# Kernel optimization log

Hardware: AMD Instinct MI355X
Metric: run time of the kernel (lower is better)

Reference implementation:

```python
import jax, jax.numpy as jnp
import numpy as np

DIM = 1024
FF = 4096
BATCH = 4
SEQ = 2048
EPS = 1e-5


def setup_inputs() -> dict:
    key = jax.random.key(0)
    ks = jax.random.split(key, 8)
    x = jax.random.normal(ks[0], (BATCH, SEQ, DIM), dtype=jnp.float32)
    # phazor init: exp(2j*pi*arange(dim)/dim) * |randn(dim)|
    ang = 2.0 * np.pi * jnp.arange(DIM, dtype=jnp.float32) / DIM
    mag = jnp.abs(jax.random.normal(ks[1], (DIM,), dtype=jnp.float32))
    phazor_re = mag * jnp.cos(ang)
    phazor_im = mag * jnp.sin(ang)
    last_re = jax.random.normal(ks[2], (DIM,), dtype=jnp.float32)
    last_im = jax.random.normal(ks[3], (DIM,), dtype=jnp.float32)
    w1 = jax.random.normal(ks[4], (FF, DIM), dtype=jnp.float32) * DIM ** -0.5
    b1 = jnp.zeros((FF,), dtype=jnp.float32)
    w2 = jax.random.normal(ks[5], (DIM, FF), dtype=jnp.float32) * FF ** -0.5
    b2 = jnp.zeros((DIM,), dtype=jnp.float32)
    return {
        'x': x,
        'ln1_w': jnp.ones((DIM,), jnp.float32), 'ln1_b': jnp.zeros((DIM,), jnp.float32),
        'ln2_w': jnp.ones((DIM,), jnp.float32), 'ln2_b': jnp.zeros((DIM,), jnp.float32),
        'sc_lin': jnp.ones((DIM,), jnp.float32),
        'phazor_re': phazor_re, 'phazor_im': phazor_im,
        'last_re': last_re, 'last_im': last_im,
        'w1': w1, 'b1': b1, 'w2': w2, 'b2': b2,
    }


def _layer_norm(x, w, b):
    mu = jnp.mean(x, axis=-1, keepdims=True)
    var = jnp.mean(jnp.square(x - mu), axis=-1, keepdims=True)
    return (x - mu) * jax.lax.rsqrt(var + EPS) * w + b


def _sconv(x, phazor_re, phazor_im, last_re, last_im):
    B, L, D = x.shape
    dtype = x.dtype
    xc = x.astype(jnp.complex64)
    p_raw = phazor_re + 1j * phazor_im
    # tanh(|p|) * exp(i*angle(p))
    p = (jnp.tanh(jnp.abs(p_raw)) * jnp.exp(1j * jnp.angle(p_raw))).astype(jnp.complex64)
    t = jnp.arange(L)[:, None]
    prog = jnp.power(p[None, :], t)            # [L, D] complex
    filt_fft = jnp.fft.fft(prog, n=2 * L, axis=0)   # [2L, D]
    x_fft = jnp.fft.fft(xc, n=2 * L, axis=1)        # [B, 2L, D]
    conv = jnp.fft.ifft(filt_fft[None] * x_fft, axis=1)[:, :L]  # [B, L, D]
    last = (last_re + 1j * last_im)[None, None, :]  # [1,1,D] broadcast over batch
    conv_with_past = conv + last * prog[None] * p[None, None]
    return conv_with_past.real.astype(dtype)


def reference(x, ln1_w, ln1_b, ln2_w, ln2_b, sc_lin,
              phazor_re, phazor_im, last_re, last_im,
              w1, b1, w2, b2):
    # SConv branch
    x_res = x
    h = _layer_norm(x, ln1_w, ln1_b)
    h = jax.nn.silu(h)
    h = _sconv(h, phazor_re, phazor_im, last_re, last_im)
    h = h * sc_lin
    x = h + x_res
    # FFN branch
    x_res = x
    h = _layer_norm(x, ln2_w, ln2_b)
    h = jax.nn.silu(jnp.einsum('bld,fd->blf', h, w1) + b1)
    h = jnp.einsum('blf,df->bld', h, w2) + b2
    return h + x_res
```

## Files before the change

### kernel.cpp

```cpp
#include <hip/hip_runtime.h>
#include <cmath>


#define DIMD 1024
#define FFD  4096
#define BATCH 4
#define SEQL 2048
#define MROWS (BATCH*SEQL)
#define EPSF 1e-5f
#define CHUNKS 32
#define CLEN (SEQL/CHUNKS)

typedef __attribute__((ext_vector_type(8))) _Float16 half8;
typedef __attribute__((ext_vector_type(4))) _Float16 half4;
typedef __attribute__((ext_vector_type(4))) float    floatx4;

#define H_OFF    0u
#define E_OFF    33554432u
#define SIN_OFF  34603008u
#define H2_OFF   35651584u
#define W1H_OFF  52428800u
#define W2H_OFF  60817408u
#define Y1_OFF   69206016u

__device__ __forceinline__ void load_lds16(const _Float16* g, _Float16* l) {
    __builtin_amdgcn_global_load_lds(
        (const __attribute__((address_space(1))) unsigned int*)g,
        (__attribute__((address_space(3))) unsigned int*)l,
        16, 0, 0);
}

__global__ __launch_bounds__(256)
void cast_f32_f16(const float* __restrict__ src, _Float16* __restrict__ dst) {
    int i = (blockIdx.x * 256 + threadIdx.x) * 4;
    float4 v = *(const float4*)(src + i);
    half4 o;
    o.x = (_Float16)v.x; o.y = (_Float16)v.y; o.z = (_Float16)v.z; o.w = (_Float16)v.w;
    *(half4*)(dst + i) = o;
}

__global__ __launch_bounds__(256)
void ln_kernel(const float* __restrict__ x, const float* __restrict__ w,
               const float* __restrict__ b, float* __restrict__ of,
               _Float16* __restrict__ oh, int mode) {
    const size_t row = blockIdx.x;
    const int tid = threadIdx.x;
    float4 v = *(const float4*)(x + row * DIMD + tid * 4);
    float s = (v.x + v.y) + (v.z + v.w);
    float q = (v.x * v.x + v.y * v.y) + (v.z * v.z + v.w * v.w);
    #pragma unroll
    for (int off = 32; off; off >>= 1) {
        s += __shfl_down(s, off, 64);
        q += __shfl_down(q, off, 64);
    }
    __shared__ float red[8];
    if (!(tid & 63)) { red[tid >> 6] = s; red[4 + (tid >> 6)] = q; }
    __syncthreads();
    s = (red[0] + red[1]) + (red[2] + red[3]);
    q = (red[4] + red[5]) + (red[6] + red[7]);
    const float mu = s * (1.f / DIMD);
    const float rs = rsqrtf(q * (1.f / DIMD) - mu * mu + EPSF);
    float4 wv = *(const float4*)(w + tid * 4);
    float4 bv = *(const float4*)(b + tid * 4);
    float o0 = (v.x - mu) * rs * wv.x + bv.x;
    float o1 = (v.y - mu) * rs * wv.y + bv.y;
    float o2 = (v.z - mu) * rs * wv.z + bv.z;
    float o3 = (v.w - mu) * rs * wv.w + bv.w;
    if (mode == 1) {
        o0 = o0 / (1.f + __expf(-o0));
        o1 = o1 / (1.f + __expf(-o1));
        o2 = o2 / (1.f + __expf(-o2));
        o3 = o3 / (1.f + __expf(-o3));
        float4 ov = {o0, o1, o2, o3};
        *(float4*)(of + row * DIMD + tid * 4) = ov;
    } else {
        half4 hv;
        hv.x = (_Float16)o0; hv.y = (_Float16)o1;
        hv.z = (_Float16)o2; hv.w = (_Float16)o3;
        *(half4*)(oh + row * DIMD + tid * 4) = hv;
    }
}

__device__ __forceinline__ void get_p(const float* pre, const float* pim, int d,
                                      float& pr, float& pi) {
    float re = pre[d], im = pim[d];
    float r = sqrtf(re * re + im * im);
    float t = tanhf(r) / fmaxf(r, 1e-30f);
    pr = re * t; pi = im * t;
}

__global__ __launch_bounds__(256)
void scan_partial(const float* __restrict__ h, const float* __restrict__ pre,
                  const float* __restrict__ pim, float2* __restrict__ e) {
    const int d = blockIdx.x * 256 + threadIdx.x;
    const int c = blockIdx.y;
    const int bb = blockIdx.z;
    float pr, pi; get_p(pre, pim, d, pr, pi);
    float sr = 0.f, si = 0.f;
    const float* hp = h + ((size_t)bb * SEQL + (size_t)c * CLEN) * DIMD + d;
    #pragma unroll 4
    for (int j = 0; j < CLEN; ++j) {
        float hv = hp[(size_t)j * DIMD];
        float nr = pr * sr - pi * si + hv;
        float ni = pr * si + pi * sr;
        sr = nr; si = ni;
    }
    e[((size_t)bb * CHUNKS + c) * DIMD + d] = make_float2(sr, si);
}

__global__ __launch_bounds__(256)
void scan_combine(const float2* __restrict__ e, const float* __restrict__ pre,
                  const float* __restrict__ pim, const float* __restrict__ lre,
                  const float* __restrict__ lim, float2* __restrict__ sv) {
    const int d = blockIdx.x * 256 + threadIdx.x;
    const int bb = blockIdx.y;
    float pr, pi; get_p(pre, pim, d, pr, pi);
    float qr = pr, qi = pi;
    #pragma unroll
    for (int s = 0; s < 6; ++s) {
        float nr = qr * qr - qi * qi;
        float ni = 2.f * qr * qi;
        qr = nr; qi = ni;
    }
    float sr = lre[d], si = lim[d];
    for (int c = 0; c < CHUNKS; ++c) {
        sv[((size_t)bb * CHUNKS + c) * DIMD + d] = make_float2(sr, si);
        float2 ec = e[((size_t)bb * CHUNKS + c) * DIMD + d];
        float nr = qr * sr - qi * si + ec.x;
        float ni = qr * si + qi * sr + ec.y;
        sr = nr; si = ni;
    }
}

__global__ __launch_bounds__(256)
void scan_final(const float* __restrict__ h, const float* __restrict__ x,
                const float* __restrict__ pre, const float* __restrict__ pim,
                const float* __restrict__ sc, const float2* __restrict__ sv,
                float* __restrict__ x2) {
    const int d = blockIdx.x * 256 + threadIdx.x;
    const int c = blockIdx.y;
    const int bb = blockIdx.z;
    float pr, pi; get_p(pre, pim, d, pr, pi);
    float2 s0 = sv[((size_t)bb * CHUNKS + c) * DIMD + d];
    float sr = s0.x, si = s0.y;
    const float scd = sc[d];
    const size_t base = ((size_t)bb * SEQL + (size_t)c * CLEN) * DIMD + d;
    #pragma unroll 4
    for (int j = 0; j < CLEN; ++j) {
        float hv = h[base + (size_t)j * DIMD];
        float nr = pr * sr - pi * si + hv;
        float ni = pr * si + pi * sr;
        sr = nr; si = ni;
        x2[base + (size_t)j * DIMD] = x[base + (size_t)j * DIMD] + scd * sr;
    }
}

#define BM 128
#define BN 128
#define BK 64

__global__ __launch_bounds__(256)
void gemm_bt(const _Float16* __restrict__ A, const _Float16* __restrict__ W,
             const float* __restrict__ bias, _Float16* __restrict__ out_h,
             const float* resid, float* out_f, int N, int K, int epi) {
    __shared__ _Float16 As[BM * BK];
    __shared__ _Float16 Bs[BN * BK];
    const int tid  = threadIdx.x;
    const int lane = tid & 63;
    const int wave = tid >> 6;
    const int wm = (wave >> 1) * 64;
    const int wn = (wave & 1) * 64;
    const size_t m0 = (size_t)blockIdx.y * BM;
    const size_t n0 = (size_t)blockIdx.x * BN;
    const int fr = lane & 15;
    const int quad = lane >> 4;

    const int srow = wave * 32 + (lane >> 3);
    const int ccp  = ((lane & 7) ^ (lane >> 3)) * 8;
    const _Float16* ag = A + (m0 + srow) * (size_t)K + ccp;
    const _Float16* wg = W + (n0 + srow) * (size_t)K + ccp;
    _Float16* asl = &As[(wave * 32) * BK];
    _Float16* bsl = &Bs[(wave * 32) * BK];

    floatx4 acc[4][4] = {};

    for (int k0 = 0; k0 < K; k0 += BK) {
        #pragma unroll
        for (int t = 0; t < 4; ++t) {
            load_lds16(ag + k0 + (size_t)(t * 8) * K, asl + t * 8 * BK);
            load_lds16(wg + k0 + (size_t)(t * 8) * K, bsl + t * 8 * BK);
        }
        __syncthreads();
        #pragma unroll
        for (int kk = 0; kk < BK; kk += 32) {
            half8 af[4], bf[4];
            #pragma unroll
            for (int i = 0; i < 4; ++i) {
                const int slot = (((kk >> 3) + quad) ^ (fr & 7)) * 8;
                af[i] = *(const half8*)(&As[(wm + i * 16 + fr) * BK + slot]);
                bf[i] = *(const half8*)(&Bs[(wn + i * 16 + fr) * BK + slot]);
            }
            #pragma unroll
            for (int i = 0; i < 4; ++i)
                #pragma unroll
                for (int j = 0; j < 4; ++j)
                    acc[i][j] = __builtin_amdgcn_mfma_f32_16x16x32_f16(
                        af[i], bf[j], acc[i][j], 0, 0, 0);
        }
        __syncthreads();
    }

    #pragma unroll
    for (int i = 0; i < 4; ++i) {
        #pragma unroll
        for (int j = 0; j < 4; ++j) {
            #pragma unroll
            for (int r = 0; r < 4; ++r) {
                const size_t gm = m0 + wm + i * 16 + quad * 4 + r;
                const size_t gn = n0 + wn + j * 16 + fr;
                float v = acc[i][j][r] + bias[gn];
                if (epi == 1) {
                    float sl = v / (1.f + __expf(-v));
                    out_h[gm * N + gn] = (_Float16)sl;
                } else {
                    out_f[gm * N + gn] = v + resid[gm * N + gn];
                }
            }
        }
    }
}

extern "C" void kernel_launch(void* const* d_in, const int* in_sizes, int n_in,
                              void* d_out, int out_size, void* d_ws, size_t ws_size,
                              hipStream_t stream) {
    const float* x    = (const float*)d_in[0];
    const float* ln1w = (const float*)d_in[1];
    const float* ln1b = (const float*)d_in[2];
    const float* ln2w = (const float*)d_in[3];
    const float* ln2b = (const float*)d_in[4];
    const float* sc   = (const float*)d_in[5];
    const float* pre  = (const float*)d_in[6];
    const float* pim  = (const float*)d_in[7];
    const float* lre  = (const float*)d_in[8];
    const float* lim  = (const float*)d_in[9];
    const float* w1   = (const float*)d_in[10];
    const float* b1   = (const float*)d_in[11];
    const float* w2   = (const float*)d_in[12];
    const float* b2   = (const float*)d_in[13];

    char* ws = (char*)d_ws;
    float*      h   = (float*)(ws + H_OFF);
    float2*     e   = (float2*)(ws + E_OFF);
    float2*     sv  = (float2*)(ws + SIN_OFF);
    _Float16*   h2  = (_Float16*)(ws + H2_OFF);
    _Float16*   w1h = (_Float16*)(ws + W1H_OFF);
    _Float16*   w2h = (_Float16*)(ws + W2H_OFF);
    _Float16*   y1  = (_Float16*)(ws + Y1_OFF);
    float*      x2  = (float*)d_out;
    float*      outp = (float*)d_out;

    cast_f32_f16<<<dim3(FFD * DIMD / 1024), 256, 0, stream>>>(w1, w1h);
    cast_f32_f16<<<dim3(FFD * DIMD / 1024), 256, 0, stream>>>(w2, w2h);
    ln_kernel<<<dim3(MROWS), 256, 0, stream>>>(x, ln1w, ln1b, h, nullptr, 1);
    scan_partial<<<dim3(DIMD / 256, CHUNKS, BATCH), 256, 0, stream>>>(h, pre, pim, e);
    scan_combine<<<dim3(DIMD / 256, BATCH), 256, 0, stream>>>(e, pre, pim, lre, lim, sv);
    scan_final<<<dim3(DIMD / 256, CHUNKS, BATCH), 256, 0, stream>>>(h, x, pre, pim, sc, sv, x2);
    ln_kernel<<<dim3(MROWS), 256, 0, stream>>>(x2, ln2w, ln2b, nullptr, h2, 2);
    gemm_bt<<<dim3(FFD / BN, MROWS / BM), 256, 0, stream>>>(
        h2, w1h, b1, y1, nullptr, nullptr, FFD, DIMD, 1);
    gemm_bt<<<dim3(DIMD / BN, MROWS / BM), 256, 0, stream>>>(
        y1, w2h, b2, nullptr, x2, outp, DIMD, FFD, 2);
}
```

Measured before the change: 385.0 us.

## Replace FFN GEMMs with 8-wave double-buffered ping-pong MFMA kernel

Replaces the simple 128x128 single-buffered GEMM with a 256-row-tile, 512-thread kernel that double-buffers LDS and interleaves global-to-LDS staging with quarter-tile MFMA phases, using explicit vmcnt waits, barriers and s_setprio. It also remaps block IDs across XCDs for L2 locality and specializes the epilogue by template. The goal is to hide memory latency and raise MFMA utilization in the two FFN GEMMs that dominate runtime. The cost is much more complex hand-scheduled synchronization that depends on exact counts of outstanding loads, and larger LDS and register use.

```diff
diff --git a/kernel.cpp b/kernel.cpp
--- a/kernel.cpp
+++ b/kernel.cpp
@@ -155,79 +155,173 @@
     }
 }
 
-#define BM 128
-#define BN 128
-#define BK 64
-
-__global__ __launch_bounds__(256)
-void gemm_bt(const _Float16* __restrict__ A, const _Float16* __restrict__ W,
-             const float* __restrict__ bias, _Float16* __restrict__ out_h,
-             const float* resid, float* out_f, int N, int K, int epi) {
-    __shared__ _Float16 As[BM * BK];
-    __shared__ _Float16 Bs[BN * BK];
+#define MEMF asm volatile("" ::: "memory")
+#define BARR do { MEMF; __builtin_amdgcn_s_barrier(); MEMF; } while (0)
+
+template<int BN, int WM, int WN, int EPI>
+__global__ __launch_bounds__(512)
+void gemm8p(const _Float16* __restrict__ A, const _Float16* __restrict__ W,
+            const float* __restrict__ bias, _Float16* __restrict__ out_h,
+            const float* resid, float* out_f, int N, int K) {
+    constexpr int BM = 256, BK = 64;
+    constexpr int RC = (BM / 2) / WM;
+    constexpr int CC = (BN / 2) / WN;
+    constexpr int FR = RC / 16;
+    constexpr int FC = CC / 16;
+    constexpr int BI = BN / 128;
+
+    __shared__ __align__(16) _Float16 As[2 * BM * BK];
+    __shared__ __align__(16) _Float16 Bs[2 * BN * BK];
+
     const int tid  = threadIdx.x;
     const int lane = tid & 63;
     const int wave = tid >> 6;
-    const int wm = (wave >> 1) * 64;
-    const int wn = (wave & 1) * 64;
-    const size_t m0 = (size_t)blockIdx.y * BM;
-    const size_t n0 = (size_t)blockIdx.x * BN;
-    const int fr = lane & 15;
+    const int fr   = lane & 15;
     const int quad = lane >> 4;
-
-    const int srow = wave * 32 + (lane >> 3);
-    const int ccp  = ((lane & 7) ^ (lane >> 3)) * 8;
-    const _Float16* ag = A + (m0 + srow) * (size_t)K + ccp;
-    const _Float16* wg = W + (n0 + srow) * (size_t)K + ccp;
-    _Float16* asl = &As[(wave * 32) * BK];
-    _Float16* bsl = &Bs[(wave * 32) * BK];
-
-    floatx4 acc[4][4] = {};
-
-    for (int k0 = 0; k0 < K; k0 += BK) {
+    const int wm   = wave / WN;
+    const int wn   = wave % WN;
+
+    const int nx  = N / BN;
+    const int nwg = nx * (MROWS / BM);
+    const int lb  = blockIdx.y * gridDim.x + blockIdx.x;
+    const int sid = (lb & 7) * (nwg >> 3) + (lb >> 3);
+    const size_t m0 = (size_t)(sid / nx) * BM;
+    const size_t n0 = (size_t)(sid % nx) * BN;
+
+    const int srow = lane >> 3;
+    const int gch  = (lane & 7) ^ srow;
+    const _Float16* Ag = A + (m0 + (size_t)(wave * 8 + srow)) * K + gch * 8;
+    const _Float16* Wg = W + (n0 + (size_t)(wave * 8 + srow)) * K + gch * 8;
+    _Float16* Asl = &As[(wave * 8) * BK];
+    _Float16* Bsl = &Bs[(wave * 8) * BK];
+
+#define STAGE_A(b, kt, h) do { \
+    load_lds16(Ag + (size_t)((h)*128 +  0) * K + (size_t)(kt) * BK, \
+               Asl + ((b)*BM + (h)*128 +  0) * BK); \
+    load_lds16(Ag + (size_t)((h)*128 + 64) * K + (size_t)(kt) * BK, \
+               Asl + ((b)*BM + (h)*128 + 64) * BK); \
+} while (0)
+
+#define STAGE_B(b, kt, h) do { \
+    load_lds16(Wg + (size_t)((h)*(BN/2) +  0) * K + (size_t)(kt) * BK, \
+               Bsl + ((b)*BN + (h)*(BN/2) +  0) * BK); \
+    if (BI == 2) \
+    load_lds16(Wg + (size_t)((h)*(BN/2) + 64) * K + (size_t)(kt) * BK, \
+               Bsl + ((b)*BN + (h)*(BN/2) + 64) * BK); \
+} while (0)
+
+    half8 Af[FR][2], Bf[FC][2];
+
+#define READ_A(b, rg) do { \
+    _Pragma("unroll") \
+    for (int f_ = 0; f_ < FR; ++f_) { \
+        const int R_ = (rg)*128 + wm*RC + f_*16 + fr; \
+        _Pragma("unroll") \
+        for (int ks_ = 0; ks_ < 2; ++ks_) { \
+            const int slot_ = (ks_*4 + quad) ^ (fr & 7); \
+            Af[f_][ks_] = *(const half8*)&As[((b)*BM + R_) * BK + slot_*8]; \
+        } \
+    } \
+} while (0)
+
+#define READ_B(b, cg) do { \
+    _Pragma("unroll") \
+    for (int j_ = 0; j_ < FC; ++j_) { \
+        const int Rb_ = (cg)*(BN/2) + wn*CC + j_*16 + fr; \
+        _Pragma("unroll") \
+        for (int ks_ = 0; ks_ < 2; ++ks_) { \
+            const int slot_ = (ks_*4 + quad) ^ (fr & 7); \
+            Bf[j_][ks_] = *(const half8*)&Bs[((b)*BN + Rb_) * BK + slot_*8]; \
+        } \
+    } \
+} while (0)
+
+#define MM(rg, cg) do { \
+    _Pragma("unroll") \
+    for (int f_ = 0; f_ < FR; ++f_) \
+    _Pragma("unroll") \
+    for (int j_ = 0; j_ < FC; ++j_) \
+    _Pragma("unroll") \
+    for (int ks_ = 0; ks_ < 2; ++ks_) \
+        acc[(rg)*FR + f_][(cg)*FC + j_] = __builtin_amdgcn_mfma_f32_16x16x32_f16( \
+            Af[f_][ks_], Bf[j_][ks_], acc[(rg)*FR + f_][(cg)*FC + j_], 0, 0, 0); \
+} while (0)
+
+#define WAIT_STEADY do { \
+    if constexpr (BN == 256) asm volatile("s_waitcnt vmcnt(6)" ::: "memory"); \
+    else                     asm volatile("s_waitcnt vmcnt(5)" ::: "memory"); \
+} while (0)
+
+    floatx4 acc[2 * FR][2 * FC] = {};
+    const int nt = K / BK;
+
+    STAGE_A(0, 0, 0);
+    STAGE_A(0, 0, 1);
+    STAGE_B(0, 0, 0);
+    STAGE_B(0, 0, 1);
+    STAGE_A(1, 1, 0);
+    STAGE_B(1, 1, 1);
+    STAGE_A(1, 1, 1);
+    WAIT_STEADY;
+    BARR;
+
+    for (int t = 0; t < nt; ++t) {
+        const int cur = t & 1;
+        const int nxt = cur ^ 1;
+        READ_A(cur, 0);
+        READ_B(cur, 0);
+        if (t + 1 < nt) STAGE_B(nxt, t + 1, 0);
+        BARR;
+        __builtin_amdgcn_s_setprio(1); MM(0, 0); __builtin_amdgcn_s_setprio(0);
+        BARR;
+        READ_B(cur, 1);
+        if (t + 2 < nt) STAGE_A(cur, t + 2, 0);
+        BARR;
+        __builtin_amdgcn_s_setprio(1); MM(0, 1); __builtin_amdgcn_s_setprio(0);
+        BARR;
+        READ_A(cur, 1);
+        if (t + 2 < nt) STAGE_B(cur, t + 2, 1);
+        BARR;
+        __builtin_amdgcn_s_setprio(1); MM(1, 1); __builtin_amdgcn_s_setprio(0);
+        BARR;
+        READ_B(cur, 0);
+        if (t + 2 < nt) STAGE_A(cur, t + 2, 1);
+        BARR;
+        __builtin_amdgcn_s_setprio(1); MM(1, 0); __builtin_amdgcn_s_setprio(0);
+        if (t < nt - 2) WAIT_STEADY;
+        else            asm volatile("s_waitcnt vmcnt(0)" ::: "memory");
+        BARR;
+    }
+
+    #pragma unroll
+    for (int rg = 0; rg < 2; ++rg)
+    #pragma unroll
+    for (int f = 0; f < FR; ++f)
+    #pragma unroll
+    for (int cg = 0; cg < 2; ++cg)
+    #pragma unroll
+    for (int j = 0; j < FC; ++j) {
+        const floatx4 a = acc[rg * FR + f][cg * FC + j];
+        const size_t gn = n0 + cg * (BN / 2) + wn * CC + j * 16 + fr;
+        const float bb = bias[gn];
         #pragma unroll
-        for (int t = 0; t < 4; ++t) {
-            load_lds16(ag + k0 + (size_t)(t * 8) * K, asl + t * 8 * BK);
-            load_lds16(wg + k0 + (size_t)(t * 8) * K, bsl + t * 8 * BK);
-        }
-        __syncthreads();
-        #pragma unroll
-        for (int kk = 0; kk < BK; kk += 32) {
-            half8 af[4], bf[4];
-            #pragma unroll
-            for (int i = 0; i < 4; ++i) {
-                const int slot = (((kk >> 3) + quad) ^ (fr & 7)) * 8;
-                af[i] = *(const half8*)(&As[(wm + i * 16 + fr) * BK + slot]);
-                bf[i] = *(const half8*)(&Bs[(wn + i * 16 + fr) * BK + slot]);
-            }
-            #pragma unroll
-            for (int i = 0; i < 4; ++i)
-                #pragma unroll
-                for (int j = 0; j < 4; ++j)
-                    acc[i][j] = __builtin_amdgcn_mfma_f32_16x16x32_f16(
-                        af[i], bf[j], acc[i][j], 0, 0, 0);
-        }
-        __syncthreads();
-    }
-
-    #pragma unroll
-    for (int i = 0; i < 4; ++i) {
-        #pragma unroll
-        for (int j = 0; j < 4; ++j) {
-            #pragma unroll
-            for (int r = 0; r < 4; ++r) {
-                const size_t gm = m0 + wm + i * 16 + quad * 4 + r;
-                const size_t gn = n0 + wn + j * 16 + fr;
-                float v = acc[i][j][r] + bias[gn];
-                if (epi == 1) {
-                    float sl = v / (1.f + __expf(-v));
-                    out_h[gm * N + gn] = (_Float16)sl;
-                } else {
-                    out_f[gm * N + gn] = v + resid[gm * N + gn];
-                }
+        for (int r = 0; r < 4; ++r) {
+            const size_t gm = m0 + rg * 128 + wm * RC + f * 16 + quad * 4 + r;
+            float v = a[r] + bb;
+            if (EPI == 1) {
+                float sl = v / (1.f + __expf(-v));
+                out_h[gm * (size_t)N + gn] = (_Float16)sl;
+            } else {
+                out_f[gm * (size_t)N + gn] = v + resid[gm * (size_t)N + gn];
             }
         }
     }
+#undef STAGE_A
+#undef STAGE_B
+#undef READ_A
+#undef READ_B
+#undef MM
+#undef WAIT_STEADY
 }
 
 extern "C" void kernel_launch(void* const* d_in, const int* in_sizes, int n_in,
@@ -266,8 +360,8 @@
     scan_combine<<<dim3(DIMD / 256, BATCH), 256, 0, stream>>>(e, pre, pim, lre, lim, sv);
     scan_final<<<dim3(DIMD / 256, CHUNKS, BATCH), 256, 0, stream>>>(h, x, pre, pim, sc, sv, x2);
     ln_kernel<<<dim3(MROWS), 256, 0, stream>>>(x2, ln2w, ln2b, nullptr, h2, 2);
-    gemm_bt<<<dim3(FFD / BN, MROWS / BM), 256, 0, stream>>>(
-        h2, w1h, b1, y1, nullptr, nullptr, FFD, DIMD, 1);
-    gemm_bt<<<dim3(DIMD / BN, MROWS / BM), 256, 0, stream>>>(
-        y1, w2h, b2, nullptr, x2, outp, DIMD, FFD, 2);
-}
+    gemm8p<256, 2, 4, 1><<<dim3(FFD / 256, MROWS / 256), 512, 0, stream>>>(
+        h2, w1h, b1, y1, nullptr, nullptr, FFD, DIMD);
+    gemm8p<128, 4, 2, 2><<<dim3(DIMD / 128, MROWS / 256), 512, 0, stream>>>(
+        y1, w2h, b2, nullptr, x2, outp, DIMD, FFD);
+}
```

After: 361.8 us. -6.0%, faster.

## Fuse layernorms into chunked scan kernels and swizzle GEMM block order

Applied to the files above, without the earlier changes.

Folds LN1+SiLU into the scan-partial pass and recomputes them in scan-final, which also applies LN2 and writes the fp16 GEMM input. This removes the fp32 intermediate h buffer and two standalone layernorm passes. The scan is restructured so one block handles a 16-row chunk across all 1024 channels, with 128 chunks instead of 32. The GEMMs get a grouped block-index swizzle for better L2 reuse. In exchange, x is read twice, the sequential combine stage is longer, and per-row block reductions add sync overhead.

```diff
diff --git a/kernel.cpp b/kernel.cpp
--- a/kernel.cpp
+++ b/kernel.cpp
@@ -8,16 +8,16 @@
 #define SEQL 2048
 #define MROWS (BATCH*SEQL)
 #define EPSF 1e-5f
-#define CHUNKS 32
-#define CLEN (SEQL/CHUNKS)
+#define CHUNKS2 128
+#define CLEN2 16
 
 typedef __attribute__((ext_vector_type(8))) _Float16 half8;
 typedef __attribute__((ext_vector_type(4))) _Float16 half4;
 typedef __attribute__((ext_vector_type(4))) float    floatx4;
 
-#define H_OFF    0u
-#define E_OFF    33554432u
-#define SIN_OFF  34603008u
+#define ST_OFF   0u
+#define E_OFF    1048576u
+#define SV_OFF   5242880u
 #define H2_OFF   35651584u
 #define W1H_OFF  52428800u
 #define W2H_OFF  60817408u
@@ -39,48 +39,6 @@
     *(half4*)(dst + i) = o;
 }
 
-__global__ __launch_bounds__(256)
-void ln_kernel(const float* __restrict__ x, const float* __restrict__ w,
-               const float* __restrict__ b, float* __restrict__ of,
-               _Float16* __restrict__ oh, int mode) {
-    const size_t row = blockIdx.x;
-    const int tid = threadIdx.x;
-    float4 v = *(const float4*)(x + row * DIMD + tid * 4);
-    float s = (v.x + v.y) + (v.z + v.w);
-    float q = (v.x * v.x + v.y * v.y) + (v.z * v.z + v.w * v.w);
-    #pragma unroll
-    for (int off = 32; off; off >>= 1) {
-        s += __shfl_down(s, off, 64);
-        q += __shfl_down(q, off, 64);
-    }
-    __shared__ float red[8];
-    if (!(tid & 63)) { red[tid >> 6] = s; red[4 + (tid >> 6)] = q; }
-    __syncthreads();
-    s = (red[0] + red[1]) + (red[2] + red[3]);
-    q = (red[4] + red[5]) + (red[6] + red[7]);
-    const float mu = s * (1.f / DIMD);
-    const float rs = rsqrtf(q * (1.f / DIMD) - mu * mu + EPSF);
-    float4 wv = *(const float4*)(w + tid * 4);
-    float4 bv = *(const float4*)(b + tid * 4);
-    float o0 = (v.x - mu) * rs * wv.x + bv.x;
-    float o1 = (v.y - mu) * rs * wv.y + bv.y;
-    float o2 = (v.z - mu) * rs * wv.z + bv.z;
-    float o3 = (v.w - mu) * rs * wv.w + bv.w;
-    if (mode == 1) {
-        o0 = o0 / (1.f + __expf(-o0));
-        o1 = o1 / (1.f + __expf(-o1));
-        o2 = o2 / (1.f + __expf(-o2));
-        o3 = o3 / (1.f + __expf(-o3));
-        float4 ov = {o0, o1, o2, o3};
-        *(float4*)(of + row * DIMD + tid * 4) = ov;
-    } else {
-        half4 hv;
-        hv.x = (_Float16)o0; hv.y = (_Float16)o1;
-        hv.z = (_Float16)o2; hv.w = (_Float16)o3;
-        *(half4*)(oh + row * DIMD + tid * 4) = hv;
-    }
-}
-
 __device__ __forceinline__ void get_p(const float* pre, const float* pim, int d,
                                       float& pr, float& pi) {
     float re = pre[d], im = pim[d];
@@ -89,23 +47,67 @@
     pr = re * t; pi = im * t;
 }
 
-__global__ __launch_bounds__(256)
-void scan_partial(const float* __restrict__ h, const float* __restrict__ pre,
-                  const float* __restrict__ pim, float2* __restrict__ e) {
-    const int d = blockIdx.x * 256 + threadIdx.x;
-    const int c = blockIdx.y;
-    const int bb = blockIdx.z;
-    float pr, pi; get_p(pre, pim, d, pr, pi);
-    float sr = 0.f, si = 0.f;
-    const float* hp = h + ((size_t)bb * SEQL + (size_t)c * CLEN) * DIMD + d;
-    #pragma unroll 4
-    for (int j = 0; j < CLEN; ++j) {
-        float hv = hp[(size_t)j * DIMD];
-        float nr = pr * sr - pi * si + hv;
-        float ni = pr * si + pi * sr;
-        sr = nr; si = ni;
-    }
-    e[((size_t)bb * CHUNKS + c) * DIMD + d] = make_float2(sr, si);
+__device__ __forceinline__ void block_red2(float& s, float& q, float (*red)[8],
+                                           int tid, int buf) {
+    #pragma unroll
+    for (int off = 32; off; off >>= 1) {
+        s += __shfl_down(s, off, 64);
+        q += __shfl_down(q, off, 64);
+    }
+    if (!(tid & 63)) { red[buf][tid >> 6] = s; red[buf][4 + (tid >> 6)] = q; }
+    __syncthreads();
+    s = (red[buf][0] + red[buf][1]) + (red[buf][2] + red[buf][3]);
+    q = (red[buf][4] + red[buf][5]) + (red[buf][6] + red[buf][7]);
+}
+
+__global__ __launch_bounds__(256)
+void scan_partial(const float* __restrict__ x, const float* __restrict__ lw,
+                  const float* __restrict__ lb, const float* __restrict__ pre,
+                  const float* __restrict__ pim, float2* __restrict__ st,
+                  float2* __restrict__ e) {
+    const int tid = threadIdx.x;
+    const int c = blockIdx.x;
+    const int bb = blockIdx.y;
+    const int d0 = tid * 4;
+    float pr[4], pi[4];
+    #pragma unroll
+    for (int k = 0; k < 4; ++k) get_p(pre, pim, d0 + k, pr[k], pi[k]);
+    const float4 wv = *(const float4*)(lw + d0);
+    const float4 bv = *(const float4*)(lb + d0);
+    const size_t row0 = (size_t)bb * SEQL + (size_t)c * CLEN2;
+
+    float4 vbuf[CLEN2];
+    #pragma unroll
+    for (int j = 0; j < CLEN2; ++j)
+        vbuf[j] = *(const float4*)(x + (row0 + j) * DIMD + d0);
+
+    __shared__ float red[2][8];
+    float sr[4] = {0.f, 0.f, 0.f, 0.f}, si[4] = {0.f, 0.f, 0.f, 0.f};
+    #pragma unroll
+    for (int j = 0; j < CLEN2; ++j) {
+        float4 v = vbuf[j];
+        float s = (v.x + v.y) + (v.z + v.w);
+        float q = (v.x * v.x + v.y * v.y) + (v.z * v.z + v.w * v.w);
+        block_red2(s, q, red, tid, j & 1);
+        const float mu = s * (1.f / DIMD);
+        const float rs = rsqrtf(q * (1.f / DIMD) - mu * mu + EPSF);
+        if (tid == 0) st[row0 + j] = make_float2(mu, rs);
+        float hv[4];
+        hv[0] = (v.x - mu) * rs * wv.x + bv.x;
+        hv[1] = (v.y - mu) * rs * wv.y + bv.y;
+        hv[2] = (v.z - mu) * rs * wv.z + bv.z;
+        hv[3] = (v.w - mu) * rs * wv.w + bv.w;
+        #pragma unroll
+        for (int k = 0; k < 4; ++k) {
+            float h = hv[k] / (1.f + __expf(-hv[k]));
+            float nr = pr[k] * sr[k] - pi[k] * si[k] + h;
+            float ni = pr[k] * si[k] + pi[k] * sr[k];
+            sr[k] = nr; si[k] = ni;
+        }
+    }
+    float2* ep = e + ((size_t)bb * CHUNKS2 + c) * DIMD + d0;
+    #pragma unroll
+    for (int k = 0; k < 4; ++k) ep[k] = make_float2(sr[k], si[k]);
 }
 
 __global__ __launch_bounds__(256)
@@ -117,15 +119,15 @@
     float pr, pi; get_p(pre, pim, d, pr, pi);
     float qr = pr, qi = pi;
     #pragma unroll
-    for (int s = 0; s < 6; ++s) {
+    for (int s = 0; s < 4; ++s) {
         float nr = qr * qr - qi * qi;
         float ni = 2.f * qr * qi;
         qr = nr; qi = ni;
     }
     float sr = lre[d], si = lim[d];
-    for (int c = 0; c < CHUNKS; ++c) {
-        sv[((size_t)bb * CHUNKS + c) * DIMD + d] = make_float2(sr, si);
-        float2 ec = e[((size_t)bb * CHUNKS + c) * DIMD + d];
+    for (int c = 0; c < CHUNKS2; ++c) {
+        sv[((size_t)bb * CHUNKS2 + c) * DIMD + d] = make_float2(sr, si);
+        float2 ec = e[((size_t)bb * CHUNKS2 + c) * DIMD + d];
         float nr = qr * sr - qi * si + ec.x;
         float ni = qr * si + qi * sr + ec.y;
         sr = nr; si = ni;
@@ -133,45 +135,100 @@
 }
 
 __global__ __launch_bounds__(256)
-void scan_final(const float* __restrict__ h, const float* __restrict__ x,
+void scan_final(const float* __restrict__ x, const float2* __restrict__ st,
+                const float* __restrict__ l1w, const float* __restrict__ l1b,
+                const float* __restrict__ l2w, const float* __restrict__ l2b,
                 const float* __restrict__ pre, const float* __restrict__ pim,
                 const float* __restrict__ sc, const float2* __restrict__ sv,
-                float* __restrict__ x2) {
-    const int d = blockIdx.x * 256 + threadIdx.x;
-    const int c = blockIdx.y;
-    const int bb = blockIdx.z;
-    float pr, pi; get_p(pre, pim, d, pr, pi);
-    float2 s0 = sv[((size_t)bb * CHUNKS + c) * DIMD + d];
-    float sr = s0.x, si = s0.y;
-    const float scd = sc[d];
-    const size_t base = ((size_t)bb * SEQL + (size_t)c * CLEN) * DIMD + d;
-    #pragma unroll 4
-    for (int j = 0; j < CLEN; ++j) {
-        float hv = h[base + (size_t)j * DIMD];
-        float nr = pr * sr - pi * si + hv;
-        float ni = pr * si + pi * sr;
-        sr = nr; si = ni;
-        x2[base + (size_t)j * DIMD] = x[base + (size_t)j * DIMD] + scd * sr;
-    }
-}
-
-#define BM 128
-#define BN 128
-#define BK 64
-
-__global__ __launch_bounds__(256)
-void gemm_bt(const _Float16* __restrict__ A, const _Float16* __restrict__ W,
-             const float* __restrict__ bias, _Float16* __restrict__ out_h,
-             const float* resid, float* out_f, int N, int K, int epi) {
-    __shared__ _Float16 As[BM * BK];
-    __shared__ _Float16 Bs[BN * BK];
+                float* __restrict__ x2, _Float16* __restrict__ h2) {
+    const int tid = threadIdx.x;
+    const int c = blockIdx.x;
+    const int bb = blockIdx.y;
+    const int d0 = tid * 4;
+    float pr[4], pi[4];
+    #pragma unroll
+    for (int k = 0; k < 4; ++k) get_p(pre, pim, d0 + k, pr[k], pi[k]);
+    const float4 w1v = *(const float4*)(l1w + d0);
+    const float4 b1v = *(const float4*)(l1b + d0);
+    const float4 w2v = *(const float4*)(l2w + d0);
+    const float4 b2v = *(const float4*)(l2b + d0);
+    const float4 scv = *(const float4*)(sc + d0);
+    const size_t row0 = (size_t)bb * SEQL + (size_t)c * CLEN2;
+
+    float sr[4], si[4];
+    {
+        const float2* s0 = sv + ((size_t)bb * CHUNKS2 + c) * DIMD + d0;
+        #pragma unroll
+        for (int k = 0; k < 4; ++k) { sr[k] = s0[k].x; si[k] = s0[k].y; }
+    }
+
+    float4 vbuf[CLEN2];
+    #pragma unroll
+    for (int j = 0; j < CLEN2; ++j)
+        vbuf[j] = *(const float4*)(x + (row0 + j) * DIMD + d0);
+
+    __shared__ float red[2][8];
+    #pragma unroll
+    for (int j = 0; j < CLEN2; ++j) {
+        float4 v = vbuf[j];
+        float2 s1 = st[row0 + j];
+        float o[4];
+        o[0] = (v.x - s1.x) * s1.y * w1v.x + b1v.x;
+        o[1] = (v.y - s1.x) * s1.y * w1v.y + b1v.y;
+        o[2] = (v.z - s1.x) * s1.y * w1v.z + b1v.z;
+        o[3] = (v.w - s1.x) * s1.y * w1v.w + b1v.w;
+        float x2v[4];
+        const float xa[4] = {v.x, v.y, v.z, v.w};
+        const float sca[4] = {scv.x, scv.y, scv.z, scv.w};
+        #pragma unroll
+        for (int k = 0; k < 4; ++k) {
+            float h = o[k] / (1.f + __expf(-o[k]));
+            float nr = pr[k] * sr[k] - pi[k] * si[k] + h;
+            float ni = pr[k] * si[k] + pi[k] * sr[k];
+            sr[k] = nr; si[k] = ni;
+            x2v[k] = xa[k] + sca[k] * nr;
+        }
+        float4 xo = {x2v[0], x2v[1], x2v[2], x2v[3]};
+        *(float4*)(x2 + (row0 + j) * DIMD + d0) = xo;
+        float s = (x2v[0] + x2v[1]) + (x2v[2] + x2v[3]);
+        float q = (x2v[0] * x2v[0] + x2v[1] * x2v[1]) +
+                  (x2v[2] * x2v[2] + x2v[3] * x2v[3]);
+        block_red2(s, q, red, tid, j & 1);
+        const float mu = s * (1.f / DIMD);
+        const float rs = rsqrtf(q * (1.f / DIMD) - mu * mu + EPSF);
+        const float w2a[4] = {w2v.x, w2v.y, w2v.z, w2v.w};
+        const float b2a[4] = {b2v.x, b2v.y, b2v.z, b2v.w};
+        half4 hv;
+        _Float16 ha[4];
+        #pragma unroll
+        for (int k = 0; k < 4; ++k)
+            ha[k] = (_Float16)((x2v[k] - mu) * rs * w2a[k] + b2a[k]);
+        hv.x = ha[0]; hv.y = ha[1]; hv.z = ha[2]; hv.w = ha[3];
+        *(half4*)(h2 + (row0 + j) * DIMD + d0) = hv;
+    }
+}
+
+#define GBM 128
+#define GBN 128
+#define GBK 64
+
+template<int NCOLS, int EPI>
+__global__ __launch_bounds__(256)
+void gemm_128(const _Float16* __restrict__ A, const _Float16* __restrict__ W,
+              const float* __restrict__ bias, _Float16* __restrict__ out_h,
+              const float* __restrict__ resid, float* __restrict__ out_f,
+              int N, int K) {
+    __shared__ _Float16 As[GBM * GBK];
+    __shared__ _Float16 Bs[GBN * GBK];
     const int tid  = threadIdx.x;
     const int lane = tid & 63;
     const int wave = tid >> 6;
     const int wm = (wave >> 1) * 64;
     const int wn = (wave & 1) * 64;
-    const size_t m0 = (size_t)blockIdx.y * BM;
-    const size_t n0 = (size_t)blockIdx.x * BN;
+    const int n  = blockIdx.y * gridDim.x + blockIdx.x;
+    const int xc = n & 7, ii = n >> 3;
+    const size_t m0 = (size_t)(xc + ((ii / NCOLS) << 3)) * GBM;
+    const size_t n0 = (size_t)(ii % NCOLS) * GBN;
     const int fr = lane & 15;
     const int quad = lane >> 4;
 
@@ -179,26 +236,26 @@
     const int ccp  = ((lane & 7) ^ (lane >> 3)) * 8;
     const _Float16* ag = A + (m0 + srow) * (size_t)K + ccp;
     const _Float16* wg = W + (n0 + srow) * (size_t)K + ccp;
-    _Float16* asl = &As[(wave * 32) * BK];
-    _Float16* bsl = &Bs[(wave * 32) * BK];
+    _Float16* asl = &As[(wave * 32) * GBK];
+    _Float16* bsl = &Bs[(wave * 32) * GBK];
 
     floatx4 acc[4][4] = {};
 
-    for (int k0 = 0; k0 < K; k0 += BK) {
+    for (int k0 = 0; k0 < K; k0 += GBK) {
         #pragma unroll
         for (int t = 0; t < 4; ++t) {
-            load_lds16(ag + k0 + (size_t)(t * 8) * K, asl + t * 8 * BK);
-            load_lds16(wg + k0 + (size_t)(t * 8) * K, bsl + t * 8 * BK);
+            load_lds16(ag + k0 + (size_t)(t * 8) * K, asl + t * 8 * GBK);
+            load_lds16(wg + k0 + (size_t)(t * 8) * K, bsl + t * 8 * GBK);
         }
         __syncthreads();
         #pragma unroll
-        for (int kk = 0; kk < BK; kk += 32) {
+        for (int kk = 0; kk < GBK; kk += 32) {
             half8 af[4], bf[4];
             #pragma unroll
             for (int i = 0; i < 4; ++i) {
                 const int slot = (((kk >> 3) + quad) ^ (fr & 7)) * 8;
-                af[i] = *(const half8*)(&As[(wm + i * 16 + fr) * BK + slot]);
-                bf[i] = *(const half8*)(&Bs[(wn + i * 16 + fr) * BK + slot]);
+                af[i] = *(const half8*)(&As[(wm + i * 16 + fr) * GBK + slot]);
+                bf[i] = *(const half8*)(&Bs[(wn + i * 16 + fr) * GBK + slot]);
             }
             #pragma unroll
             for (int i = 0; i < 4; ++i)
@@ -219,11 +276,11 @@
                 const size_t gm = m0 + wm + i * 16 + quad * 4 + r;
                 const size_t gn = n0 + wn + j * 16 + fr;
                 float v = acc[i][j][r] + bias[gn];
-                if (epi == 1) {
+                if (EPI == 1) {
                     float sl = v / (1.f + __expf(-v));
-                    out_h[gm * N + gn] = (_Float16)sl;
+                    out_h[gm * (size_t)N + gn] = (_Float16)sl;
                 } else {
-                    out_f[gm * N + gn] = v + resid[gm * N + gn];
+                    out_f[gm * (size_t)N + gn] = v + resid[gm * (size_t)N + gn];
                 }
             }
         }
@@ -249,9 +306,9 @@
     const float* b2   = (const float*)d_in[13];
 
     char* ws = (char*)d_ws;
-    float*      h   = (float*)(ws + H_OFF);
+    float2*     st  = (float2*)(ws + ST_OFF);
     float2*     e   = (float2*)(ws + E_OFF);
-    float2*     sv  = (float2*)(ws + SIN_OFF);
+    float2*     sv  = (float2*)(ws + SV_OFF);
     _Float16*   h2  = (_Float16*)(ws + H2_OFF);
     _Float16*   w1h = (_Float16*)(ws + W1H_OFF);
     _Float16*   w2h = (_Float16*)(ws + W2H_OFF);
@@ -261,13 +318,14 @@
 
     cast_f32_f16<<<dim3(FFD * DIMD / 1024), 256, 0, stream>>>(w1, w1h);
     cast_f32_f16<<<dim3(FFD * DIMD / 1024), 256, 0, stream>>>(w2, w2h);
-    ln_kernel<<<dim3(MROWS), 256, 0, stream>>>(x, ln1w, ln1b, h, nullptr, 1);
-    scan_partial<<<dim3(DIMD / 256, CHUNKS, BATCH), 256, 0, stream>>>(h, pre, pim, e);
-    scan_combine<<<dim3(DIMD / 256, BATCH), 256, 0, stream>>>(e, pre, pim, lre, lim, sv);
-    scan_final<<<dim3(DIMD / 256, CHUNKS, BATCH), 256, 0, stream>>>(h, x, pre, pim, sc, sv, x2);
-    ln_kernel<<<dim3(MROWS), 256, 0, stream>>>(x2, ln2w, ln2b, nullptr, h2, 2);
-    gemm_bt<<<dim3(FFD / BN, MROWS / BM), 256, 0, stream>>>(
-        h2, w1h, b1, y1, nullptr, nullptr, FFD, DIMD, 1);
-    gemm_bt<<<dim3(DIMD / BN, MROWS / BM), 256, 0, stream>>>(
-        y1, w2h, b2, nullptr, x2, outp, DIMD, FFD, 2);
-}
+    scan_partial<<<dim3(CHUNKS2, BATCH), 256, 0, stream>>>(
+        x, ln1w, ln1b, pre, pim, st, e);
+    scan_combine<<<dim3(DIMD / 256, BATCH), 256, 0, stream>>>(
+        e, pre, pim, lre, lim, sv);
+    scan_final<<<dim3(CHUNKS2, BATCH), 256, 0, stream>>>(
+        x, st, ln1w, ln1b, ln2w, ln2b, pre, pim, sc, sv, x2, h2);
+    gemm_128<32, 1><<<dim3(FFD / GBN, MROWS / GBM), 256, 0, stream>>>(
+        h2, w1h, b1, y1, nullptr, nullptr, FFD, DIMD);
+    gemm_128<8, 2><<<dim3(DIMD / GBN, MROWS / GBM), 256, 0, stream>>>(
+        y1, w2h, b2, nullptr, x2, outp, DIMD, FFD);
+}
```

Result: faster. 358.8 us (-6.8%).
